# Optimization experiments

Hardware: AMD Instinct MI355X
Metric: run time of the kernel (lower is better)

Reference implementation:

```python
import jax, jax.numpy as jnp
import numpy as np

BLANK = 0
SMOOTHING = 0.1
NEG = jnp.float32(-1e30)  # finite stand-in for -inf (grad-safe)

T, B, C, L = 1024, 128, 256, 64


def setup_inputs() -> dict:
    key = jax.random.key(0)
    k1, k2, k3, k4 = jax.random.split(key, 4)
    raw = jax.random.normal(k1, (T, B, C), dtype=jnp.float32)
    log_probs = jax.nn.log_softmax(raw, axis=-1)  # [T,B,C], valid log-softmax
    targets = jax.random.randint(k2, (B, L), 1, C)          # labels in [1,C), never blank
    input_lengths = jax.random.randint(k3, (B,), T // 2, T + 1)
    target_lengths = jax.random.randint(k4, (B,), L // 2, L + 1)
    return {"log_probs": log_probs, "targets": targets,
            "input_lengths": input_lengths, "target_lengths": target_lengths}


def _ctc_nll(log_probs, targets, input_lengths, target_lengths):
    """Per-sample CTC negative log-likelihood (reduction='none'), log-space DP."""
    Tt, Bb, Cc = log_probs.shape
    Ll = targets.shape[1]
    S = 2 * Ll + 1
    # Extended label sequence: blank, t1, blank, t2, ..., blank  -> [B,S]
    ext = jnp.full((Bb, S), BLANK, dtype=targets.dtype).at[:, 1::2].set(targets)
    ext_m2 = jnp.pad(ext[:, :-2], ((0, 0), (2, 0)), constant_values=BLANK)
    allow2 = (ext != BLANK) & (ext != ext_m2)  # skip transition allowed [B,S]
    # Gather log_probs at extended labels for all t: [T,B,S]
    lp_ext = jnp.take_along_axis(log_probs, jnp.broadcast_to(ext[None], (Tt, Bb, S)), axis=2)

    def end_ll(alpha, tl):
        # logsumexp of alpha at s = 2*tl and 2*tl-1 (final blank / final label)
        a1 = jnp.take_along_axis(alpha, (2 * tl)[:, None], axis=1)[:, 0]
        a0 = jnp.take_along_axis(alpha, (2 * tl - 1)[:, None], axis=1)[:, 0]
        m = jnp.maximum(a1, a0)
        return m + jnp.log(jnp.exp(a1 - m) + jnp.exp(a0 - m))

    alpha0 = jnp.full((Bb, S), NEG, dtype=log_probs.dtype)
    alpha0 = alpha0.at[:, 0].set(lp_ext[0, :, 0]).at[:, 1].set(lp_ext[0, :, 1])
    ll0 = jnp.where(input_lengths == 1, end_ll(alpha0, target_lengths), NEG)

    def step(carry, xs):
        alpha, ll = carry
        lp_t, t = xs
        prev1 = jnp.pad(alpha[:, :-1], ((0, 0), (1, 0)), constant_values=NEG)
        prev2 = jnp.pad(alpha[:, :-2], ((0, 0), (2, 0)), constant_values=NEG)
        prev2 = jnp.where(allow2, prev2, NEG)
        m = jnp.maximum(alpha, jnp.maximum(prev1, prev2))
        lse = m + jnp.log(jnp.exp(alpha - m) + jnp.exp(prev1 - m) + jnp.exp(prev2 - m))
        alpha_new = lse + lp_t
        ll_new = jnp.where(t == input_lengths - 1, end_ll(alpha_new, target_lengths), ll)
        return (alpha_new, ll_new), None

    (_, ll), _ = jax.lax.scan(step, (alpha0, ll0), (lp_ext[1:], jnp.arange(1, Tt)))
    nll = -ll
    # zero_infinity=True: zero out non-finite (sentinel-huge) losses
    return jnp.where(nll > 1e29, 0.0, nll)


def reference(log_probs, targets, input_lengths, target_lengths):
    ctc = _ctc_nll(log_probs, targets, input_lengths, target_lengths)  # [B]
    # Entropy-based smoothing term over all (t, b) positions
    entropy = -(jnp.exp(log_probs) * log_probs).sum(axis=2)  # [T,B]
    smooth_loss = -entropy.mean()
    return (1.0 - SMOOTHING) * ctc.mean() + SMOOTHING * smooth_loss
```

## Files before the change

### kernel.cpp

```cpp
#include <hip/hip_runtime.h>

#define NEG (-1e30f)
#define LOG2E 1.4426950408889634f
#define LN2 0.69314718055994531f
constexpr int T = 1024;
constexpr int B = 128;
constexpr int C = 256;
constexpr int L = 64;
constexpr int ENT_GRID = 1024;
constexpr int K = 16;

#if __has_builtin(__builtin_amdgcn_exp2f)
__device__ __forceinline__ float fexp2(float x) { return __builtin_amdgcn_exp2f(x); }
#else
__device__ __forceinline__ float fexp2(float x) { return __expf(x * LN2); }
#endif
#if __has_builtin(__builtin_amdgcn_logf)
__device__ __forceinline__ float flog2(float x) { return __builtin_amdgcn_logf(x); }
#else
__device__ __forceinline__ float flog2(float x) { return __logf(x) * LOG2E; }
#endif

__device__ __forceinline__ float dpp_shr1(float x, float oldv) {
  return __int_as_float(__builtin_amdgcn_update_dpp(
      __float_as_int(oldv), __float_as_int(x), 0x138, 0xF, 0xF, false));
}

#define DECL17(P)                                                           \
  float P##0, P##1, P##2, P##3, P##4, P##5, P##6, P##7, P##8, P##9, P##10,  \
      P##11, P##12, P##13, P##14, P##15, P##b;

#define LOAD1(P, c_, k_)                                                    \
  {                                                                         \
    const int t_ = min(1 + (c_)*K + k_, lenm1); \
    const unsigned off_ = labBase + ((unsigned)t_ << 17);                   \
    asm volatile("global_load_dword %0, %1, %2"                             \
                 : "=v"(P##k_)                                              \
                 : "v"(off_), "s"(lp));                                     \
  }

#define ISSUE(P, c_)                                                        \
  do {                                                                      \
    LOAD1(P, c_, 0) LOAD1(P, c_, 1) LOAD1(P, c_, 2) LOAD1(P, c_, 3)         \
    LOAD1(P, c_, 4) LOAD1(P, c_, 5) LOAD1(P, c_, 6) LOAD1(P, c_, 7)         \
    LOAD1(P, c_, 8) LOAD1(P, c_, 9) LOAD1(P, c_, 10) LOAD1(P, c_, 11)       \
    LOAD1(P, c_, 12) LOAD1(P, c_, 13) LOAD1(P, c_, 14) LOAD1(P, c_, 15)     \
    {                                                                       \
      const int tb_ = min(1 + (c_)*K + lane, lenm1);                        \
      const unsigned offb_ = blkBase + ((unsigned)tb_ << 17);               \
      asm volatile("global_load_dword %0, %1, %2"                           \
                   : "=v"(P##b)                                             \
                   : "v"(offb_), "s"(lp));                                  \
    }                                                                       \
  } while (0)

#define WAITTIE(P)                                                          \
  asm volatile("s_waitcnt vmcnt(17)"                                        \
               : "+v"(P##0), "+v"(P##1), "+v"(P##2), "+v"(P##3),            \
                 "+v"(P##4), "+v"(P##5), "+v"(P##6), "+v"(P##7),            \
                 "+v"(P##8), "+v"(P##9), "+v"(P##10), "+v"(P##11),          \
                 "+v"(P##12), "+v"(P##13), "+v"(P##14), "+v"(P##15),        \
                 "+v"(P##b))

#define STEP(P, k_)                                                         \
  if (k_ < kend_) {                                                         \
    const float sb_ = __int_as_float(                                       \
        __builtin_amdgcn_readlane(__float_as_int(blsc_), k_));              \
    const float lw_ = P##k_ * LOG2E;                                        \
    const float ev2_ = dpp_shr1(v, a0);                      \
    const float od2_ = dpp_shr1(o, NEG);                   \
    const float p2_ = sameAsPrev ? NEG : od2_;                              \
    const float m1_ = fmaxf(o, fmaxf(ev2_, p2_));                           \
    const float s1_ =                                                       \
        fexp2(o - m1_) + fexp2(ev2_ - m1_) + fexp2(p2_ - m1_);              \
    const float no_ = m1_ + flog2(s1_) + lw_;                               \
    const float m0_ = fmaxf(v, o);                                          \
    const float s0_ = fexp2(v - m0_) + fexp2(o - m0_);                      \
    const float nv_ = m0_ + flog2(s0_) + sb_;                               \
    a0 += sb_;                                                              \
    o = no_;                                                                \
    v = nv_;                                                                \
  }

#define COMPUTE(P, c_)                                                      \
  do {                                                                      \
    const float blsc_ = (P##b)*LOG2E;                                       \
    const int kend_ = steps - (c_)*K;                                       \
    STEP(P, 0) STEP(P, 1) STEP(P, 2) STEP(P, 3) STEP(P, 4) STEP(P, 5)       \
    STEP(P, 6) STEP(P, 7) STEP(P, 8) STEP(P, 9) STEP(P, 10) STEP(P, 11)     \
    STEP(P, 12) STEP(P, 13) STEP(P, 14) STEP(P, 15)                         \
  } while (0)

__global__ __launch_bounds__(256, 1) void k_fused(
    const float* __restrict__ lp, const int* __restrict__ targets,
    const int* __restrict__ in_len, const int* __restrict__ tg_len,
    float* __restrict__ ent_part, float* __restrict__ nll_out) {
  __shared__ float wsum[4];
  const int tid = threadIdx.x;

  if (blockIdx.x < ENT_GRID) {
    const size_t N4 = (size_t)T * B * C / 4;
    const float4* lp4 = (const float4*)lp;
    const size_t stride = (size_t)ENT_GRID * 256;
    float a0 = 0.f, a1 = 0.f, a2 = 0.f, a3 = 0.f;
    for (size_t i = (size_t)blockIdx.x * 256 + tid; i < N4; i += stride) {
      const float4 vv = lp4[i];
      a0 += vv.x * __expf(vv.x);
      a1 += vv.y * __expf(vv.y);
      a2 += vv.z * __expf(vv.z);
      a3 += vv.w * __expf(vv.w);
    }
    float ent = (a0 + a1) + (a2 + a3);
    for (int off = 32; off > 0; off >>= 1) ent += __shfl_down(ent, off, 64);
    if ((tid & 63) == 0) wsum[tid >> 6] = ent;
    __syncthreads();
    if (tid == 0) ent_part[blockIdx.x] = wsum[0] + wsum[1] + wsum[2] + wsum[3];
    return;
  }

  if (tid >= 64) return;
  const int b = blockIdx.x - ENT_GRID;
  const int lane = tid;
  const int len = in_len[b];
  const int tl = tg_len[b];
  const int lenm1 = len - 1;
  const int steps = lenm1;
  const int nch = (steps + K - 1) / K;

  const int cls = targets[b * L + lane];
  const int prevc = (lane == 0) ? -1 : targets[b * L + lane - 1];
  const bool sameAsPrev = (cls == prevc);
  const unsigned labBase = ((unsigned)b << 10) + ((unsigned)cls << 2);
  const unsigned blkBase = ((unsigned)b << 10);

  const float lpb0 = lp[(size_t)b * C];
  const float lpl0 = lp[(size_t)b * C + cls];
  float a0 = lpb0 * LOG2E;
  float o = (lane == 0) ? lpl0 * LOG2E : NEG;
  float v = NEG;

  asm volatile("s_waitcnt vmcnt(0) lgkmcnt(0)" ::: "memory");

  DECL17(A)
  DECL17(B)
  ISSUE(A, 0);
  int c = 0;
  for (;;) {
    ISSUE(B, c + 1);
    WAITTIE(A);
    COMPUTE(A, c);
    ++c;
    if (c == nch) break;
    ISSUE(A, c + 1);
    WAITTIE(B);
    COMPUTE(B, c);
    ++c;
    if (c == nch) break;
  }
  asm volatile("s_waitcnt vmcnt(0)" ::: "memory");

  const float aE = __shfl(v, tl - 1, 64);
  const float aO = __shfl(o, tl - 1, 64);
  if (lane == 0) {
    const float m = fmaxf(aE, aO);
    const float ll = (m + flog2(fexp2(aE - m) + fexp2(aO - m))) * LN2;
    float nll = -ll;
    if (nll > 1e29f) nll = 0.f;
    nll_out[b] = nll;
  }
}

__global__ __launch_bounds__(256) void k_final(
    const float* __restrict__ ent_part, const float* __restrict__ nll,
    float* __restrict__ out) {
  const int tid = threadIdx.x;
  float s = 0.f;
  for (int i = tid; i < ENT_GRID; i += 256) s += ent_part[i];
  float n = (tid < B) ? nll[tid] : 0.f;
  for (int off = 32; off > 0; off >>= 1) {
    s += __shfl_down(s, off, 64);
    n += __shfl_down(n, off, 64);
  }
  __shared__ float ss[4], nn[4];
  if ((tid & 63) == 0) { ss[tid >> 6] = s; nn[tid >> 6] = n; }
  __syncthreads();
  if (tid == 0) {
    const float ent_sum = ss[0] + ss[1] + ss[2] + ss[3];
    const float nll_sum = nn[0] + nn[1] + nn[2] + nn[3];
    const float ctc_mean = nll_sum / (float)B;
    const float smooth = ent_sum / (float)(T * B);
    out[0] = 0.9f * ctc_mean + 0.1f * smooth;
  }
}

extern "C" void kernel_launch(void* const* d_in, const int* in_sizes, int n_in,
                              void* d_out, int out_size, void* d_ws, size_t ws_size,
                              hipStream_t stream) {
  const float* lp      = (const float*)d_in[0];
  const int*   targets = (const int*)d_in[1];
  const int*   in_len  = (const int*)d_in[2];
  const int*   tg_len  = (const int*)d_in[3];
  float* out = (float*)d_out;
  float* ws  = (float*)d_ws;

  float* ent_part = ws;
  float* nllb     = ws + ENT_GRID;

  k_fused<<<ENT_GRID + B, 256, 0, stream>>>(lp, targets, in_len, tg_len,
                                            ent_part, nllb);
  k_final<<<1, 256, 0, stream>>>(ent_part, nllb, out);
}
```

Baseline: 240.5 us.

## Split CTC recursion into concurrent forward and backward waves meeting at midpoint

Each sample's CTC DP now uses two wavefronts. One runs the forward alpha recursion up to the middle time step while the other runs a backward beta recursion from the end. The two are combined at the midpoint with a block-wide logsumexp over all states, which roughly halves the serial dependency chain per sample. This adds LDS exchange, two barriers and a reduction, doubles the active waves, and increases the numerical complexity of the combination.

Result: faster. 212.2 us (median of 2 runs) (-11.8%).

```diff
diff --git a/kernel.cpp b/kernel.cpp
--- a/kernel.cpp
+++ b/kernel.cpp
@@ -25,32 +25,56 @@
   return __int_as_float(__builtin_amdgcn_update_dpp(
       __float_as_int(oldv), __float_as_int(x), 0x138, 0xF, 0xF, false));
 }
+__device__ __forceinline__ float dpp_shl1(float x, float oldv) {
+  return __int_as_float(__builtin_amdgcn_update_dpp(
+      __float_as_int(oldv), __float_as_int(x), 0x130, 0xF, 0xF, false));
+}
+__device__ __forceinline__ float lse2(float a, float b) {
+  return fmaxf(a, b) + flog2(1.f + fexp2(-fabsf(a - b)));
+}
 
 #define DECL17(P)                                                           \
   float P##0, P##1, P##2, P##3, P##4, P##5, P##6, P##7, P##8, P##9, P##10,  \
       P##11, P##12, P##13, P##14, P##15, P##b;
 
-#define LOAD1(P, c_, k_)                                                    \
+#define LOADF(P, c_, k_)                                                    \
   {                                                                         \
-    const int t_ = min(1 + (c_)*K + k_, lenm1); \
+    const int t_ = min(1 + (c_)*K + k_, m);     \
     const unsigned off_ = labBase + ((unsigned)t_ << 17);                   \
     asm volatile("global_load_dword %0, %1, %2"                             \
-                 : "=v"(P##k_)                                              \
-                 : "v"(off_), "s"(lp));                                     \
-  }
-
-#define ISSUE(P, c_)                                                        \
+                 : "=v"(P##k_) : "v"(off_), "s"(lp));                       \
+  }
+#define LOADB(P, c_, k_)                                                    \
+  {                                                                         \
+    const int t_ = max(len - 2 - ((c_)*K + k_), 0);                         \
+    const unsigned off_ = labBase + ((unsigned)t_ << 17);                   \
+    asm volatile("global_load_dword %0, %1, %2"                             \
+                 : "=v"(P##k_) : "v"(off_), "s"(lp));                       \
+  }
+#define ISSUEF(P, c_)                                                       \
   do {                                                                      \
-    LOAD1(P, c_, 0) LOAD1(P, c_, 1) LOAD1(P, c_, 2) LOAD1(P, c_, 3)         \
-    LOAD1(P, c_, 4) LOAD1(P, c_, 5) LOAD1(P, c_, 6) LOAD1(P, c_, 7)         \
-    LOAD1(P, c_, 8) LOAD1(P, c_, 9) LOAD1(P, c_, 10) LOAD1(P, c_, 11)       \
-    LOAD1(P, c_, 12) LOAD1(P, c_, 13) LOAD1(P, c_, 14) LOAD1(P, c_, 15)     \
+    LOADF(P, c_, 0) LOADF(P, c_, 1) LOADF(P, c_, 2) LOADF(P, c_, 3)         \
+    LOADF(P, c_, 4) LOADF(P, c_, 5) LOADF(P, c_, 6) LOADF(P, c_, 7)         \
+    LOADF(P, c_, 8) LOADF(P, c_, 9) LOADF(P, c_, 10) LOADF(P, c_, 11)       \
+    LOADF(P, c_, 12) LOADF(P, c_, 13) LOADF(P, c_, 14) LOADF(P, c_, 15)     \
     {                                                                       \
-      const int tb_ = min(1 + (c_)*K + lane, lenm1);                        \
+      const int tb_ = min(1 + (c_)*K + lane, m);                            \
       const unsigned offb_ = blkBase + ((unsigned)tb_ << 17);               \
       asm volatile("global_load_dword %0, %1, %2"                           \
-                   : "=v"(P##b)                                             \
-                   : "v"(offb_), "s"(lp));                                  \
+                   : "=v"(P##b) : "v"(offb_), "s"(lp));                     \
+    }                                                                       \
+  } while (0)
+#define ISSUEB(P, c_)                                                       \
+  do {                                                                      \
+    LOADB(P, c_, 0) LOADB(P, c_, 1) LOADB(P, c_, 2) LOADB(P, c_, 3)         \
+    LOADB(P, c_, 4) LOADB(P, c_, 5) LOADB(P, c_, 6) LOADB(P, c_, 7)         \
+    LOADB(P, c_, 8) LOADB(P, c_, 9) LOADB(P, c_, 10) LOADB(P, c_, 11)       \
+    LOADB(P, c_, 12) LOADB(P, c_, 13) LOADB(P, c_, 14) LOADB(P, c_, 15)     \
+    {                                                                       \
+      const int tb_ = max(len - 2 - (c_)*K - lane, 0);                      \
+      const unsigned offb_ = blkBase + ((unsigned)tb_ << 17);               \
+      asm volatile("global_load_dword %0, %1, %2"                           \
+                   : "=v"(P##b) : "v"(offb_), "s"(lp));                     \
     }                                                                       \
   } while (0)
 
@@ -62,33 +86,56 @@
                  "+v"(P##12), "+v"(P##13), "+v"(P##14), "+v"(P##15),        \
                  "+v"(P##b))
 
-#define STEP(P, k_)                                                         \
+#define STEPF(P, k_)                                                        \
   if (k_ < kend_) {                                                         \
     const float sb_ = __int_as_float(                                       \
         __builtin_amdgcn_readlane(__float_as_int(blsc_), k_));              \
     const float lw_ = P##k_ * LOG2E;                                        \
-    const float ev2_ = dpp_shr1(v, a0);                      \
+    const float ev2_ = dpp_shr1(v, a0);                    \
     const float od2_ = dpp_shr1(o, NEG);                   \
     const float p2_ = sameAsPrev ? NEG : od2_;                              \
     const float m1_ = fmaxf(o, fmaxf(ev2_, p2_));                           \
     const float s1_ =                                                       \
         fexp2(o - m1_) + fexp2(ev2_ - m1_) + fexp2(p2_ - m1_);              \
     const float no_ = m1_ + flog2(s1_) + lw_;                               \
-    const float m0_ = fmaxf(v, o);                                          \
-    const float s0_ = fexp2(v - m0_) + fexp2(o - m0_);                      \
-    const float nv_ = m0_ + flog2(s0_) + sb_;                               \
+    const float nv_ = lse2(v, o) + sb_;                                     \
     a0 += sb_;                                                              \
     o = no_;                                                                \
     v = nv_;                                                                \
   }
-
-#define COMPUTE(P, c_)                                                      \
+#define STEPB(P, k_)                                                        \
+  if (k_ < kend_) {                                                         \
+    const float sb_ = __int_as_float(                                       \
+        __builtin_amdgcn_readlane(__float_as_int(blsc_), k_));              \
+    const float lw_ = P##k_ * LOG2E;                                        \
+    const float es_ = dpp_shl1(eb, a0b); \
+    const float os_ = dpp_shl1(ob, NEG);                    \
+    const float p2_ = allowB ? os_ : NEG;                                   \
+    const float m1_ = fmaxf(ob, fmaxf(es_, p2_));                           \
+    const float s1_ =                                                       \
+        fexp2(ob - m1_) + fexp2(es_ - m1_) + fexp2(p2_ - m1_);              \
+    const float no_ = m1_ + flog2(s1_) + lw_;                               \
+    const float ne_ = lse2(eb, ob) + sb_;                                   \
+    a0b += sb_;                                                             \
+    ob = no_;                                                               \
+    eb = ne_;                                                               \
+  }
+
+#define COMPUTEF(P, c_)                                                     \
   do {                                                                      \
     const float blsc_ = (P##b)*LOG2E;                                       \
-    const int kend_ = steps - (c_)*K;                                       \
-    STEP(P, 0) STEP(P, 1) STEP(P, 2) STEP(P, 3) STEP(P, 4) STEP(P, 5)       \
-    STEP(P, 6) STEP(P, 7) STEP(P, 8) STEP(P, 9) STEP(P, 10) STEP(P, 11)     \
-    STEP(P, 12) STEP(P, 13) STEP(P, 14) STEP(P, 15)                         \
+    const int kend_ = stepsN - (c_)*K;                                      \
+    STEPF(P, 0) STEPF(P, 1) STEPF(P, 2) STEPF(P, 3) STEPF(P, 4) STEPF(P, 5) \
+    STEPF(P, 6) STEPF(P, 7) STEPF(P, 8) STEPF(P, 9) STEPF(P, 10)            \
+    STEPF(P, 11) STEPF(P, 12) STEPF(P, 13) STEPF(P, 14) STEPF(P, 15)        \
+  } while (0)
+#define COMPUTEB(P, c_)                                                     \
+  do {                                                                      \
+    const float blsc_ = (P##b)*LOG2E;                                       \
+    const int kend_ = stepsN - (c_)*K;                                      \
+    STEPB(P, 0) STEPB(P, 1) STEPB(P, 2) STEPB(P, 3) STEPB(P, 4) STEPB(P, 5) \
+    STEPB(P, 6) STEPB(P, 7) STEPB(P, 8) STEPB(P, 9) STEPB(P, 10)            \
+    STEPB(P, 11) STEPB(P, 12) STEPB(P, 13) STEPB(P, 14) STEPB(P, 15)        \
   } while (0)
 
 __global__ __launch_bounds__(256, 1) void k_fused(
@@ -96,6 +143,7 @@
     const int* __restrict__ in_len, const int* __restrict__ tg_len,
     float* __restrict__ ent_part, float* __restrict__ nll_out) {
   __shared__ float wsum[4];
+  __shared__ float Ast[129], Bst[129], red[4];
   const int tid = threadIdx.x;
 
   if (blockIdx.x < ENT_GRID) {
@@ -118,52 +166,103 @@
     return;
   }
 
-  if (tid >= 64) return;
+  if (tid >= 128) return;
   const int b = blockIdx.x - ENT_GRID;
-  const int lane = tid;
+  const int wave = tid >> 6;
+  const int lane = tid & 63;
   const int len = in_len[b];
   const int tl = tg_len[b];
-  const int lenm1 = len - 1;
-  const int steps = lenm1;
-  const int nch = (steps + K - 1) / K;
+  const int m = (len - 1) >> 1;
 
   const int cls = targets[b * L + lane];
-  const int prevc = (lane == 0) ? -1 : targets[b * L + lane - 1];
-  const bool sameAsPrev = (cls == prevc);
   const unsigned labBase = ((unsigned)b << 10) + ((unsigned)cls << 2);
   const unsigned blkBase = ((unsigned)b << 10);
 
-  const float lpb0 = lp[(size_t)b * C];
-  const float lpl0 = lp[(size_t)b * C + cls];
-  float a0 = lpb0 * LOG2E;
-  float o = (lane == 0) ? lpl0 * LOG2E : NEG;
-  float v = NEG;
-
-  asm volatile("s_waitcnt vmcnt(0) lgkmcnt(0)" ::: "memory");
-
-  DECL17(A)
-  DECL17(B)
-  ISSUE(A, 0);
-  int c = 0;
-  for (;;) {
-    ISSUE(B, c + 1);
-    WAITTIE(A);
-    COMPUTE(A, c);
-    ++c;
-    if (c == nch) break;
-    ISSUE(A, c + 1);
-    WAITTIE(B);
-    COMPUTE(B, c);
-    ++c;
-    if (c == nch) break;
-  }
-  asm volatile("s_waitcnt vmcnt(0)" ::: "memory");
-
-  const float aE = __shfl(v, tl - 1, 64);
-  const float aO = __shfl(o, tl - 1, 64);
-  if (lane == 0) {
-    const float m = fmaxf(aE, aO);
-    const float ll = (m + flog2(fexp2(aE - m) + fexp2(aO - m))) * LN2;
+  DECL17(X)
+  DECL17(Y)
+
+  if (wave == 0) {
+    const int stepsN = m;
+    const int nch = (stepsN + K - 1) / K;
+    const int prevc = (lane == 0) ? -1 : targets[b * L + lane - 1];
+    const bool sameAsPrev = (cls == prevc);
+    const float lpb0 = lp[(size_t)b * C];
+    const float lpl0 = lp[(size_t)b * C + cls];
+    float a0 = lpb0 * LOG2E;
+    float o = (lane == 0) ? lpl0 * LOG2E : NEG;
+    float v = NEG;
+    asm volatile("s_waitcnt vmcnt(0) lgkmcnt(0)" ::: "memory");
+    ISSUEF(X, 0);
+    int c = 0;
+    for (;;) {
+      ISSUEF(Y, c + 1);
+      WAITTIE(X);
+      COMPUTEF(X, c);
+      ++c;
+      if (c == nch) break;
+      ISSUEF(X, c + 1);
+      WAITTIE(Y);
+      COMPUTEF(Y, c);
+      ++c;
+      if (c == nch) break;
+    }
+    asm volatile("s_waitcnt vmcnt(0)" ::: "memory");
+    if (lane == 0) Ast[0] = a0;
+    Ast[2 * lane + 1] = o;
+    Ast[2 * lane + 2] = v;
+  } else {
+    const int stepsN = len - 1 - m;
+    const int nch = (stepsN + K - 1) / K;
+    const int nxtc = targets[b * L + min(lane + 1, L - 1)];
+    const bool allowB = (lane < 63) && (nxtc != cls);
+    const size_t rowE = (size_t)(len - 1) * (B * C) + (size_t)b * C;
+    const float lpbE = lp[rowE] * LOG2E;
+    const float lplE = lp[rowE + cls] * LOG2E;
+    float a0b = (tl == L) ? lpbE : NEG;
+    float ob = (lane == tl - 1) ? lplE : NEG;
+    float eb = (lane == tl && tl < L) ? lpbE : NEG;
+    asm volatile("s_waitcnt vmcnt(0) lgkmcnt(0)" ::: "memory");
+    ISSUEB(X, 0);
+    int c = 0;
+    for (;;) {
+      ISSUEB(Y, c + 1);
+      WAITTIE(X);
+      COMPUTEB(X, c);
+      ++c;
+      if (c == nch) break;
+      ISSUEB(X, c + 1);
+      WAITTIE(Y);
+      COMPUTEB(Y, c);
+      ++c;
+      if (c == nch) break;
+    }
+    asm volatile("s_waitcnt vmcnt(0)" ::: "memory");
+    if (lane == 0) Bst[128] = a0b;
+    Bst[2 * lane + 1] = ob;
+    Bst[2 * lane] = eb;
+  }
+  __syncthreads();
+
+  const size_t rowM = (size_t)m * (B * C) + (size_t)b * C;
+  const int scls = (tid & 1) ? targets[b * L + (tid >> 1)] : 0;
+  float val = Ast[tid] + Bst[tid] - lp[rowM + scls] * LOG2E;
+  if (tid == 0) {
+    const float v128 = Ast[128] + Bst[128] - lp[rowM] * LOG2E;
+    const float mm = fmaxf(val, v128);
+    val = mm + flog2(fexp2(val - mm) + fexp2(v128 - mm));
+  }
+  float mx = val;
+  for (int off = 32; off > 0; off >>= 1)
+    mx = fmaxf(mx, __shfl_xor(mx, off, 64));
+  if (lane == 0) red[wave] = mx;
+  __syncthreads();
+  mx = fmaxf(red[0], red[1]);
+  float ex = fexp2(val - mx);
+  for (int off = 32; off > 0; off >>= 1) ex += __shfl_xor(ex, off, 64);
+  if (lane == 0) red[2 + wave] = ex;
+  __syncthreads();
+  if (tid == 0) {
+    const float ll = (mx + flog2(red[2] + red[3])) * LN2;
     float nll = -ll;
     if (nll > 1e29f) nll = 0.f;
     nll_out[b] = nll;
```
